# Kernel optimization log

Measured on AMD Instinct MI355X. Metric: run time of the kernel, lower is better.

## Reference

```python
import jax, jax.numpy as jnp
import numpy as np

VOCAB = 50000
EMB = 32
HID = 32
NUM_CLASSES = 2


def setup_inputs() -> dict:
    key = jax.random.key(0)
    ks = jax.random.split(key, 8)
    B, S = 1024, 512
    x = jax.random.randint(ks[0], (B, S), 0, VOCAB, dtype=jnp.int64)
    # embedding table has vocab_size + 1 rows, per `len(encoder.vocab) + 1`
    emb = jax.random.normal(ks[1], (VOCAB + 1, EMB), dtype=jnp.float32)
    s = 1.0 / np.sqrt(HID)
    w_ih = jax.random.uniform(ks[2], (4 * HID, EMB), jnp.float32, -s, s)
    w_hh = jax.random.uniform(ks[3], (4 * HID, HID), jnp.float32, -s, s)
    b_ih = jax.random.uniform(ks[4], (4 * HID,), jnp.float32, -s, s)
    b_hh = jax.random.uniform(ks[5], (4 * HID,), jnp.float32, -s, s)
    sf = 1.0 / np.sqrt(HID)
    fc_w = jax.random.uniform(ks[6], (NUM_CLASSES, HID), jnp.float32, -sf, sf)
    fc_b = jax.random.uniform(ks[7], (NUM_CLASSES,), jnp.float32, -sf, sf)
    return {"x": x, "emb": emb, "w_ih": w_ih, "w_hh": w_hh,
            "b_ih": b_ih, "b_hh": b_hh, "fc_w": fc_w, "fc_b": fc_b}


def _lstm_last_h(x, emb, w_ih, w_hh, b_ih, b_hh):
    xe = emb[x]                                        # [B, S, EMB]
    # precompute input-to-gate projection for all timesteps: [B, S, 4H]
    xp = jnp.einsum('bse,ge->bsg', xe, w_ih) + (b_ih + b_hh)
    B = x.shape[0]
    h0 = jnp.zeros((B, HID), xp.dtype)
    c0 = jnp.zeros((B, HID), xp.dtype)

    def step(carry, xt):
        h, c = carry
        gates = xt + h @ w_hh.T                        # [B, 4H]
        i, f, g, o = jnp.split(gates, 4, axis=-1)      # PyTorch gate order
        i = jax.nn.sigmoid(i)
        f = jax.nn.sigmoid(f)
        g = jnp.tanh(g)
        o = jax.nn.sigmoid(o)
        c = f * c + i * g
        h = o * jnp.tanh(c)
        return (h, c), None

    (h_n, c_n), _ = jax.lax.scan(step, (h0, c0), jnp.swapaxes(xp, 0, 1))
    return h_n                                          # last-timestep hidden


def reference(x, emb, w_ih, w_hh, b_ih, b_hh, fc_w, fc_b):
    h_last = _lstm_last_h(x, emb, w_ih, w_hh, b_ih, b_hh)
    return h_last @ fc_w.T + fc_b                       # [B, 2]
```

## Files before the change

### kernel.cpp

```cpp
#include <hip/hip_runtime.h>


#define LOG2E 1.44269504088896340736f

typedef float f32x8 __attribute__((ext_vector_type(8)));

__device__ __forceinline__ float fast_rcp(float x) { return __builtin_amdgcn_rcpf(x); }
__device__ __forceinline__ float fast_exp2(float x) { return __builtin_amdgcn_exp2f(x); }

__device__ __forceinline__ float lane_bcast(float v, int srclane) {
    return __uint_as_float(__builtin_amdgcn_readlane(__float_as_uint(v), srclane));
}

__device__ __forceinline__ float bcast_hi(float x) {
#if __has_builtin(__builtin_amdgcn_permlane32_swap)
    typedef unsigned uv2 __attribute__((ext_vector_type(2)));
    uv2 r = __builtin_amdgcn_permlane32_swap(__float_as_uint(x), __float_as_uint(x),
                                             false, false);
    return __uint_as_float(r.y);
#else
    return __shfl_xor(x, 32, 64);
#endif
}

__global__ __launch_bounds__(64, 1) void build_ptab(
    const float4* __restrict__ emb4, const float4* __restrict__ wih4,
    const float* __restrict__ bih, const float* __restrict__ bhh,
    float2* __restrict__ ptab, int nrows) {
    const int lane = threadIdx.x;

    float w0[32], w1[32];
#pragma unroll
    for (int q = 0; q < 8; ++q) {
        float4 a = wih4[lane * 8 + q];
        float4 b = wih4[(lane + 64) * 8 + q];
        w0[4 * q + 0] = a.x; w0[4 * q + 1] = a.y; w0[4 * q + 2] = a.z; w0[4 * q + 3] = a.w;
        w1[4 * q + 0] = b.x; w1[4 * q + 1] = b.y; w1[4 * q + 2] = b.z; w1[4 * q + 3] = b.w;
    }
    const float bias0 = bih[lane] + bhh[lane];
    const float bias1 = bih[lane + 64] + bhh[lane + 64];
    const float s0 = -LOG2E;
    const float s1 = (lane < 32) ? (2.0f * LOG2E) : (-LOG2E);

    for (int v = blockIdx.x; v < nrows; v += gridDim.x) {
        float a0 = bias0, a1 = bias1;
#pragma unroll
        for (int q = 0; q < 8; ++q) {
            float4 e = emb4[v * 8 + q];
            a0 = fmaf(e.x, w0[4 * q + 0], a0);
            a0 = fmaf(e.y, w0[4 * q + 1], a0);
            a0 = fmaf(e.z, w0[4 * q + 2], a0);
            a0 = fmaf(e.w, w0[4 * q + 3], a0);
            a1 = fmaf(e.x, w1[4 * q + 0], a1);
            a1 = fmaf(e.y, w1[4 * q + 1], a1);
            a1 = fmaf(e.z, w1[4 * q + 2], a1);
            a1 = fmaf(e.w, w1[4 * q + 3], a1);
        }
        ptab[v * 64 + lane] = make_float2(a0 * s0, a1 * s1);
    }
}

#define DOT8(WA, WB, XACC, YACC, JB)                                          \
    do {                                                                      \
        float _h0 = lane_bcast(h, (JB) + 0);                                  \
        float _h1 = lane_bcast(h, (JB) + 1);                                  \
        float _h2 = lane_bcast(h, (JB) + 2);                                  \
        float _h3 = lane_bcast(h, (JB) + 3);                                  \
        float _h4 = lane_bcast(h, (JB) + 4);                                  \
        float _h5 = lane_bcast(h, (JB) + 5);                                  \
        float _h6 = lane_bcast(h, (JB) + 6);                                  \
        float _h7 = lane_bcast(h, (JB) + 7);                                  \
        XACC = fmaf(_h0, WA[0], XACC); YACC = fmaf(_h0, WB[0], YACC);         \
        XACC = fmaf(_h1, WA[1], XACC); YACC = fmaf(_h1, WB[1], YACC);         \
        XACC = fmaf(_h2, WA[2], XACC); YACC = fmaf(_h2, WB[2], YACC);         \
        XACC = fmaf(_h3, WA[3], XACC); YACC = fmaf(_h3, WB[3], YACC);         \
        XACC = fmaf(_h4, WA[4], XACC); YACC = fmaf(_h4, WB[4], YACC);         \
        XACC = fmaf(_h5, WA[5], XACC); YACC = fmaf(_h5, WB[5], YACC);         \
        XACC = fmaf(_h6, WA[6], XACC); YACC = fmaf(_h6, WB[6], YACC);         \
        XACC = fmaf(_h7, WA[7], XACC); YACC = fmaf(_h7, WB[7], YACC);         \
    } while (0)

#define STEP(G0, G1)                                                          \
    do {                                                                      \
        float _x0 = (G0), _x1 = 0.f, _x2 = 0.f, _x3 = 0.f;                    \
        float _y0 = (G1), _y1 = 0.f, _y2 = 0.f, _y3 = 0.f;                    \
        DOT8(wA0, wB0, _x0, _y0, 0);                                          \
        DOT8(wA1, wB1, _x1, _y1, 8);                                          \
        DOT8(wA2, wB2, _x2, _y2, 16);                                         \
        DOT8(wA3, wB3, _x3, _y3, 24);                                         \
        float _a0 = (_x0 + _x1) + (_x2 + _x3);    \
        float _a1 = (_y0 + _y1) + (_y2 + _y3);    \
        float _sg = fast_rcp(1.0f + fast_exp2(_a0));        \
        float _r1 = fast_rcp(1.0f + fast_exp2(_a1));               \
        float _fg = bcast_hi(_sg);                                            \
        float _og = bcast_hi(_r1);                                            \
        float _gg = fmaf(-2.0f, _r1, 1.0f);                  \
        c = fmaf(_fg, c, _sg * _gg);                                          \
        float _e2 = fast_exp2(c * (2.0f * LOG2E));                            \
        h = _og * fmaf(-2.0f, fast_rcp(1.0f + _e2), 1.0f);                    \
    } while (0)

template <bool PTAB>
__global__ __launch_bounds__(64, 1) void lstm_scan(
    const int* __restrict__ x,
    const float2* __restrict__ ptab,
    const float* __restrict__ emb,
    const float* __restrict__ wih,
    const float* __restrict__ bih,
    const float* __restrict__ bhh,
    const float* __restrict__ whh,
    const float* __restrict__ fcw,
    const float* __restrict__ fcb,
    float* __restrict__ out,
    int S) {
    extern __shared__ int xrow[];
    const int b = blockIdx.x;
    const int lane = threadIdx.x;

    for (int i = lane; i < S + 16; i += 64) xrow[i] = (i < S) ? x[(size_t)b * S + i] : 0;
    __syncthreads();

    const float s0 = -LOG2E;
    const float s1 = (lane < 32) ? (2.0f * LOG2E) : (-LOG2E);

    f32x8 wA0, wA1, wA2, wA3, wB0, wB1, wB2, wB3;
    {
        const float4* whh4 = (const float4*)whh;
#pragma unroll
        for (int q = 0; q < 2; ++q) {
            float4 a = whh4[lane * 8 + q];
            float4 bb = whh4[(lane + 64) * 8 + q];
            wA0[4 * q + 0] = a.x * s0;  wA0[4 * q + 1] = a.y * s0;
            wA0[4 * q + 2] = a.z * s0;  wA0[4 * q + 3] = a.w * s0;
            wB0[4 * q + 0] = bb.x * s1; wB0[4 * q + 1] = bb.y * s1;
            wB0[4 * q + 2] = bb.z * s1; wB0[4 * q + 3] = bb.w * s1;
        }
#pragma unroll
        for (int q = 0; q < 2; ++q) {
            float4 a = whh4[lane * 8 + 2 + q];
            float4 bb = whh4[(lane + 64) * 8 + 2 + q];
            wA1[4 * q + 0] = a.x * s0;  wA1[4 * q + 1] = a.y * s0;
            wA1[4 * q + 2] = a.z * s0;  wA1[4 * q + 3] = a.w * s0;
            wB1[4 * q + 0] = bb.x * s1; wB1[4 * q + 1] = bb.y * s1;
            wB1[4 * q + 2] = bb.z * s1; wB1[4 * q + 3] = bb.w * s1;
        }
#pragma unroll
        for (int q = 0; q < 2; ++q) {
            float4 a = whh4[lane * 8 + 4 + q];
            float4 bb = whh4[(lane + 64) * 8 + 4 + q];
            wA2[4 * q + 0] = a.x * s0;  wA2[4 * q + 1] = a.y * s0;
            wA2[4 * q + 2] = a.z * s0;  wA2[4 * q + 3] = a.w * s0;
            wB2[4 * q + 0] = bb.x * s1; wB2[4 * q + 1] = bb.y * s1;
            wB2[4 * q + 2] = bb.z * s1; wB2[4 * q + 3] = bb.w * s1;
        }
#pragma unroll
        for (int q = 0; q < 2; ++q) {
            float4 a = whh4[lane * 8 + 6 + q];
            float4 bb = whh4[(lane + 64) * 8 + 6 + q];
            wA3[4 * q + 0] = a.x * s0;  wA3[4 * q + 1] = a.y * s0;
            wA3[4 * q + 2] = a.z * s0;  wA3[4 * q + 3] = a.w * s0;
            wB3[4 * q + 0] = bb.x * s1; wB3[4 * q + 1] = bb.y * s1;
            wB3[4 * q + 2] = bb.z * s1; wB3[4 * q + 3] = bb.w * s1;
        }
    }
    asm volatile("" : "+v"(wA0), "+v"(wA1), "+v"(wA2), "+v"(wA3),
                      "+v"(wB0), "+v"(wB1), "+v"(wB2), "+v"(wB3));

    float h = 0.0f, c = 0.0f;

    if constexpr (PTAB) {
        int i0 = xrow[4], i1 = xrow[5], i2 = xrow[6], i3 = xrow[7];
        float2 p0 = ptab[(size_t)xrow[0] * 64 + lane];
        float2 p1 = ptab[(size_t)xrow[1] * 64 + lane];
        float2 p2 = ptab[(size_t)xrow[2] * 64 + lane];
        float2 p3 = ptab[(size_t)xrow[3] * 64 + lane];
        int t = 0;
        for (; t + 8 <= S; t += 4) {
            STEP(p0.x, p0.y); p0 = ptab[(size_t)i0 * 64 + lane]; i0 = xrow[t + 8];
            STEP(p1.x, p1.y); p1 = ptab[(size_t)i1 * 64 + lane]; i1 = xrow[t + 9];
            STEP(p2.x, p2.y); p2 = ptab[(size_t)i2 * 64 + lane]; i2 = xrow[t + 10];
            STEP(p3.x, p3.y); p3 = ptab[(size_t)i3 * 64 + lane]; i3 = xrow[t + 11];
        }
        if (t + 0 < S) STEP(p0.x, p0.y);
        if (t + 1 < S) STEP(p1.x, p1.y);
        if (t + 2 < S) STEP(p2.x, p2.y);
        if (t + 3 < S) STEP(p3.x, p3.y);
        if (t + 4 < S) { float2 q = ptab[(size_t)i0 * 64 + lane]; STEP(q.x, q.y); }
        if (t + 5 < S) { float2 q = ptab[(size_t)i1 * 64 + lane]; STEP(q.x, q.y); }
        if (t + 6 < S) { float2 q = ptab[(size_t)i2 * 64 + lane]; STEP(q.x, q.y); }
    } else {
        f32x8 wiA0, wiA1, wiB0, wiB1;
        {
            const float4* wih4 = (const float4*)wih;
#pragma unroll
            for (int q = 0; q < 4; ++q) {
                float4 a = wih4[lane * 8 + q];
                float4 bb = wih4[(lane + 64) * 8 + q];
                float* dst0 = (q < 2) ? (float*)&wiA0 : (float*)&wiA1;
                float* dst1 = (q < 2) ? (float*)&wiB0 : (float*)&wiB1;
                int o = (q & 1) * 4;
                dst0[o + 0] = a.x * s0;  dst0[o + 1] = a.y * s0;
                dst0[o + 2] = a.z * s0;  dst0[o + 3] = a.w * s0;
                dst1[o + 0] = bb.x * s1; dst1[o + 1] = bb.y * s1;
                dst1[o + 2] = bb.z * s1; dst1[o + 3] = bb.w * s1;
            }
        }
        f32x8 wiA2, wiA3, wiB2, wiB3;
        {
            const float4* wih4 = (const float4*)wih;
#pragma unroll
            for (int q = 4; q < 8; ++q) {
                float4 a = wih4[lane * 8 + q];
                float4 bb = wih4[(lane + 64) * 8 + q];
                float* dst0 = (q < 6) ? (float*)&wiA2 : (float*)&wiA3;
                float* dst1 = (q < 6) ? (float*)&wiB2 : (float*)&wiB3;
                int o = (q & 1) * 4;
                dst0[o + 0] = a.x * s0;  dst0[o + 1] = a.y * s0;
                dst0[o + 2] = a.z * s0;  dst0[o + 3] = a.w * s0;
                dst1[o + 0] = bb.x * s1; dst1[o + 1] = bb.y * s1;
                dst1[o + 2] = bb.z * s1; dst1[o + 3] = bb.w * s1;
            }
        }
        const float bias0 = (bih[lane] + bhh[lane]) * s0;
        const float bias1 = (bih[lane + 64] + bhh[lane + 64]) * s1;
        const float4* emb4 = (const float4*)emb;
        for (int t = 0; t < S; ++t) {
            int idx = xrow[t];
            float a0 = bias0, a1 = bias1;
#pragma unroll
            for (int q = 0; q < 2; ++q) {
                float4 e = emb4[(size_t)idx * 8 + q];
                a0 = fmaf(e.x, wiA0[4 * q + 0], a0); a0 = fmaf(e.y, wiA0[4 * q + 1], a0);
                a0 = fmaf(e.z, wiA0[4 * q + 2], a0); a0 = fmaf(e.w, wiA0[4 * q + 3], a0);
                a1 = fmaf(e.x, wiB0[4 * q + 0], a1); a1 = fmaf(e.y, wiB0[4 * q + 1], a1);
                a1 = fmaf(e.z, wiB0[4 * q + 2], a1); a1 = fmaf(e.w, wiB0[4 * q + 3], a1);
            }
#pragma unroll
            for (int q = 0; q < 2; ++q) {
                float4 e = emb4[(size_t)idx * 8 + 2 + q];
                a0 = fmaf(e.x, wiA1[4 * q + 0], a0); a0 = fmaf(e.y, wiA1[4 * q + 1], a0);
                a0 = fmaf(e.z, wiA1[4 * q + 2], a0); a0 = fmaf(e.w, wiA1[4 * q + 3], a0);
                a1 = fmaf(e.x, wiB1[4 * q + 0], a1); a1 = fmaf(e.y, wiB1[4 * q + 1], a1);
                a1 = fmaf(e.z, wiB1[4 * q + 2], a1); a1 = fmaf(e.w, wiB1[4 * q + 3], a1);
            }
#pragma unroll
            for (int q = 0; q < 2; ++q) {
                float4 e = emb4[(size_t)idx * 8 + 4 + q];
                a0 = fmaf(e.x, wiA2[4 * q + 0], a0); a0 = fmaf(e.y, wiA2[4 * q + 1], a0);
                a0 = fmaf(e.z, wiA2[4 * q + 2], a0); a0 = fmaf(e.w, wiA2[4 * q + 3], a0);
                a1 = fmaf(e.x, wiB2[4 * q + 0], a1); a1 = fmaf(e.y, wiB2[4 * q + 1], a1);
                a1 = fmaf(e.z, wiB2[4 * q + 2], a1); a1 = fmaf(e.w, wiB2[4 * q + 3], a1);
            }
#pragma unroll
            for (int q = 0; q < 2; ++q) {
                float4 e = emb4[(size_t)idx * 8 + 6 + q];
                a0 = fmaf(e.x, wiA3[4 * q + 0], a0); a0 = fmaf(e.y, wiA3[4 * q + 1], a0);
                a0 = fmaf(e.z, wiA3[4 * q + 2], a0); a0 = fmaf(e.w, wiA3[4 * q + 3], a0);
                a1 = fmaf(e.x, wiB3[4 * q + 0], a1); a1 = fmaf(e.y, wiB3[4 * q + 1], a1);
                a1 = fmaf(e.z, wiB3[4 * q + 2], a1); a1 = fmaf(e.w, wiB3[4 * q + 3], a1);
            }
            STEP(a0, a1);
        }
    }

    float wv0 = fcw[lane & 31];
    float wv1 = fcw[32 + (lane & 31)];
    float p0v = (lane < 32) ? h * wv0 : 0.0f;
    float p1v = (lane < 32) ? h * wv1 : 0.0f;
#pragma unroll
    for (int m = 32; m >= 1; m >>= 1) {
        p0v += __shfl_xor(p0v, m, 64);
        p1v += __shfl_xor(p1v, m, 64);
    }
    if (lane == 0) {
        out[b * 2 + 0] = p0v + fcb[0];
        out[b * 2 + 1] = p1v + fcb[1];
    }
}

extern "C" void kernel_launch(void* const* d_in, const int* in_sizes, int n_in,
                              void* d_out, int out_size, void* d_ws, size_t ws_size,
                              hipStream_t stream) {
    const int* x = (const int*)d_in[0];
    const float* emb = (const float*)d_in[1];
    const float* wih = (const float*)d_in[2];
    const float* whh = (const float*)d_in[3];
    const float* bih = (const float*)d_in[4];
    const float* bhh = (const float*)d_in[5];
    const float* fcw = (const float*)d_in[6];
    const float* fcb = (const float*)d_in[7];
    float* out = (float*)d_out;

    const int B = out_size / 2;
    const int S = in_sizes[0] / B;
    const int nrows = in_sizes[1] / 32;

    const size_t need = (size_t)nrows * 64 * sizeof(float2);
    const size_t smem = (size_t)(S + 16) * sizeof(int);

    if (ws_size >= need) {
        float2* ptab = (float2*)d_ws;
        int nb = nrows < 4096 ? nrows : 4096;
        build_ptab<<<nb, 64, 0, stream>>>((const float4*)emb, (const float4*)wih,
                                          bih, bhh, ptab, nrows);
        lstm_scan<true><<<B, 64, smem, stream>>>(x, ptab, emb, wih, bih, bhh, whh,
                                                 fcw, fcb, out, S);
    } else {
        lstm_scan<false><<<B, 64, smem, stream>>>(x, nullptr, emb, wih, bih, bhh, whh,
                                                  fcw, fcb, out, S);
    }
}
```

Baseline: 169.9 us.

## Replace readlane broadcasts with DPP wave rotation for the recurrent matvec

Each step no longer broadcasts all 32 hidden values through scalar readlane. The hidden vector is now rotated across the wavefront one lane at a time with a DPP move, and each lane holds its W_hh row pre-permuted to match the rotation order. The rotation direction is probed at runtime. The gate exchange between the two half-waves uses shfl_xor with selects instead of permlane32_swap. The aim is to avoid the SGPR round-trip and its hazards, at the cost of one serial 32-deep rotate+FMA chain with a single accumulator per output. It also relies on the wave-rotate DPP mode behaving as expected on this chip.

```diff
diff --git a/kernel.cpp b/kernel.cpp
--- a/kernel.cpp
+++ b/kernel.cpp
@@ -8,19 +8,8 @@
 __device__ __forceinline__ float fast_rcp(float x) { return __builtin_amdgcn_rcpf(x); }
 __device__ __forceinline__ float fast_exp2(float x) { return __builtin_amdgcn_exp2f(x); }
 
-__device__ __forceinline__ float lane_bcast(float v, int srclane) {
-    return __uint_as_float(__builtin_amdgcn_readlane(__float_as_uint(v), srclane));
-}
-
-__device__ __forceinline__ float bcast_hi(float x) {
-#if __has_builtin(__builtin_amdgcn_permlane32_swap)
-    typedef unsigned uv2 __attribute__((ext_vector_type(2)));
-    uv2 r = __builtin_amdgcn_permlane32_swap(__float_as_uint(x), __float_as_uint(x),
-                                             false, false);
-    return __uint_as_float(r.y);
-#else
-    return __shfl_xor(x, 32, 64);
-#endif
+__device__ __forceinline__ float rot1(float v) {
+    return __int_as_float(__builtin_amdgcn_mov_dpp(__float_as_int(v), 0x13C, 0xF, 0xF, true));
 }
 
 __global__ __launch_bounds__(64, 1) void build_ptab(
@@ -60,44 +49,41 @@
     }
 }
 
-#define DOT8(WA, WB, XACC, YACC, JB)                                          \
-    do {                                                                      \
-        float _h0 = lane_bcast(h, (JB) + 0);                                  \
-        float _h1 = lane_bcast(h, (JB) + 1);                                  \
-        float _h2 = lane_bcast(h, (JB) + 2);                                  \
-        float _h3 = lane_bcast(h, (JB) + 3);                                  \
-        float _h4 = lane_bcast(h, (JB) + 4);                                  \
-        float _h5 = lane_bcast(h, (JB) + 5);                                  \
-        float _h6 = lane_bcast(h, (JB) + 6);                                  \
-        float _h7 = lane_bcast(h, (JB) + 7);                                  \
-        XACC = fmaf(_h0, WA[0], XACC); YACC = fmaf(_h0, WB[0], YACC);         \
-        XACC = fmaf(_h1, WA[1], XACC); YACC = fmaf(_h1, WB[1], YACC);         \
-        XACC = fmaf(_h2, WA[2], XACC); YACC = fmaf(_h2, WB[2], YACC);         \
-        XACC = fmaf(_h3, WA[3], XACC); YACC = fmaf(_h3, WB[3], YACC);         \
-        XACC = fmaf(_h4, WA[4], XACC); YACC = fmaf(_h4, WB[4], YACC);         \
-        XACC = fmaf(_h5, WA[5], XACC); YACC = fmaf(_h5, WB[5], YACC);         \
-        XACC = fmaf(_h6, WA[6], XACC); YACC = fmaf(_h6, WB[6], YACC);         \
-        XACC = fmaf(_h7, WA[7], XACC); YACC = fmaf(_h7, WB[7], YACC);         \
-    } while (0)
-
-#define STEP(G0, G1)                                                          \
-    do {                                                                      \
-        float _x0 = (G0), _x1 = 0.f, _x2 = 0.f, _x3 = 0.f;                    \
-        float _y0 = (G1), _y1 = 0.f, _y2 = 0.f, _y3 = 0.f;                    \
-        DOT8(wA0, wB0, _x0, _y0, 0);                                          \
-        DOT8(wA1, wB1, _x1, _y1, 8);                                          \
-        DOT8(wA2, wB2, _x2, _y2, 16);                                         \
-        DOT8(wA3, wB3, _x3, _y3, 24);                                         \
-        float _a0 = (_x0 + _x1) + (_x2 + _x3);    \
-        float _a1 = (_y0 + _y1) + (_y2 + _y3);    \
-        float _sg = fast_rcp(1.0f + fast_exp2(_a0));        \
-        float _r1 = fast_rcp(1.0f + fast_exp2(_a1));               \
-        float _fg = bcast_hi(_sg);                                            \
-        float _og = bcast_hi(_r1);                                            \
-        float _gg = fmaf(-2.0f, _r1, 1.0f);                  \
-        c = fmaf(_fg, c, _sg * _gg);                                          \
-        float _e2 = fast_exp2(c * (2.0f * LOG2E));                            \
-        h = _og * fmaf(-2.0f, fast_rcp(1.0f + _e2), 1.0f);                    \
+#define REP32(M) M(0) M(1) M(2) M(3) M(4) M(5) M(6) M(7) M(8) M(9) M(10) M(11) \
+    M(12) M(13) M(14) M(15) M(16) M(17) M(18) M(19) M(20) M(21) M(22) M(23)    \
+    M(24) M(25) M(26) M(27) M(28) M(29) M(30) M(31)
+
+#define WDECL(N) float wa##N, wb##N;
+#define WLOAD(N)                                                   \
+    {                                                              \
+        int _col = (lane + dir * ((N) + 1)) & 31;                  \
+        wa##N = whh[lane * 32 + _col] * s0;                        \
+        wb##N = whh[(lane + 64) * 32 + _col] * s1;                 \
+    }
+#define WPIN(N) asm volatile("" : "+v"(wa##N), "+v"(wb##N));
+
+#define RF(N)                                                      \
+    _hr = rot1(_hr);                                               \
+    _a0 = fmaf(_hr, wa##N, _a0);                                   \
+    _a1 = fmaf(_hr, wb##N, _a1);
+
+#define STEP(G0, G1)                                                           \
+    do {                                                                       \
+        float _a0 = (G0), _a1 = (G1);                                          \
+        float _hr = h;                                                         \
+        REP32(RF)                                                              \
+        float _sg = fast_rcp(1.0f + fast_exp2(_a0));  \
+        float _r1 = fast_rcp(1.0f + fast_exp2(_a1));  \
+        float _sgx = __shfl_xor(_sg, 32, 64);                                  \
+        float _r1x = __shfl_xor(_r1, 32, 64);                                  \
+        float _ig = lo ? _sg : _sgx;                                           \
+        float _fg = lo ? _sgx : _sg;                                           \
+        float _rg = lo ? _r1 : _r1x;                                           \
+        float _og = lo ? _r1x : _r1;                                           \
+        float _gg = fmaf(-2.0f, _rg, 1.0f);          \
+        c = fmaf(_fg, c, _ig * _gg);                                           \
+        float _th = fmaf(-2.0f, fast_rcp(1.0f + fast_exp2(c * (2.0f * LOG2E))), 1.0f); \
+        h = _og * _th;                                                         \
     } while (0)
 
 template <bool PTAB>
@@ -116,55 +102,23 @@
     extern __shared__ int xrow[];
     const int b = blockIdx.x;
     const int lane = threadIdx.x;
+    const bool lo = lane < 32;
 
     for (int i = lane; i < S + 16; i += 64) xrow[i] = (i < S) ? x[(size_t)b * S + i] : 0;
     __syncthreads();
 
     const float s0 = -LOG2E;
-    const float s1 = (lane < 32) ? (2.0f * LOG2E) : (-LOG2E);
-
-    f32x8 wA0, wA1, wA2, wA3, wB0, wB1, wB2, wB3;
+    const float s1 = lo ? (2.0f * LOG2E) : (-LOG2E);
+
+    int dir;
     {
-        const float4* whh4 = (const float4*)whh;
-#pragma unroll
-        for (int q = 0; q < 2; ++q) {
-            float4 a = whh4[lane * 8 + q];
-            float4 bb = whh4[(lane + 64) * 8 + q];
-            wA0[4 * q + 0] = a.x * s0;  wA0[4 * q + 1] = a.y * s0;
-            wA0[4 * q + 2] = a.z * s0;  wA0[4 * q + 3] = a.w * s0;
-            wB0[4 * q + 0] = bb.x * s1; wB0[4 * q + 1] = bb.y * s1;
-            wB0[4 * q + 2] = bb.z * s1; wB0[4 * q + 3] = bb.w * s1;
-        }
-#pragma unroll
-        for (int q = 0; q < 2; ++q) {
-            float4 a = whh4[lane * 8 + 2 + q];
-            float4 bb = whh4[(lane + 64) * 8 + 2 + q];
-            wA1[4 * q + 0] = a.x * s0;  wA1[4 * q + 1] = a.y * s0;
-            wA1[4 * q + 2] = a.z * s0;  wA1[4 * q + 3] = a.w * s0;
-            wB1[4 * q + 0] = bb.x * s1; wB1[4 * q + 1] = bb.y * s1;
-            wB1[4 * q + 2] = bb.z * s1; wB1[4 * q + 3] = bb.w * s1;
-        }
-#pragma unroll
-        for (int q = 0; q < 2; ++q) {
-            float4 a = whh4[lane * 8 + 4 + q];
-            float4 bb = whh4[(lane + 64) * 8 + 4 + q];
-            wA2[4 * q + 0] = a.x * s0;  wA2[4 * q + 1] = a.y * s0;
-            wA2[4 * q + 2] = a.z * s0;  wA2[4 * q + 3] = a.w * s0;
-            wB2[4 * q + 0] = bb.x * s1; wB2[4 * q + 1] = bb.y * s1;
-            wB2[4 * q + 2] = bb.z * s1; wB2[4 * q + 3] = bb.w * s1;
-        }
-#pragma unroll
-        for (int q = 0; q < 2; ++q) {
-            float4 a = whh4[lane * 8 + 6 + q];
-            float4 bb = whh4[(lane + 64) * 8 + 6 + q];
-            wA3[4 * q + 0] = a.x * s0;  wA3[4 * q + 1] = a.y * s0;
-            wA3[4 * q + 2] = a.z * s0;  wA3[4 * q + 3] = a.w * s0;
-            wB3[4 * q + 0] = bb.x * s1; wB3[4 * q + 1] = bb.y * s1;
-            wB3[4 * q + 2] = bb.z * s1; wB3[4 * q + 3] = bb.w * s1;
-        }
-    }
-    asm volatile("" : "+v"(wA0), "+v"(wA1), "+v"(wA2), "+v"(wA3),
-                      "+v"(wB0), "+v"(wB1), "+v"(wB2), "+v"(wB3));
+        int got = __builtin_amdgcn_mov_dpp(lane, 0x13C, 0xF, 0xF, true);
+        dir = (got == ((lane + 1) & 63)) ? 1 : -1;
+    }
+
+    REP32(WDECL)
+    REP32(WLOAD)
+    REP32(WPIN)
 
     float h = 0.0f, c = 0.0f;
 
@@ -265,8 +219,8 @@
 
     float wv0 = fcw[lane & 31];
     float wv1 = fcw[32 + (lane & 31)];
-    float p0v = (lane < 32) ? h * wv0 : 0.0f;
-    float p1v = (lane < 32) ? h * wv1 : 0.0f;
+    float p0v = lo ? h * wv0 : 0.0f;
+    float p1v = lo ? h * wv1 : 0.0f;
 #pragma unroll
     for (int m = 32; m >= 1; m >>= 1) {
         p0v += __shfl_xor(p0v, m, 64);
```

Result: slower. 197.7 us (+16.4%).
